# Performance work log

Hardware: AMD Instinct MI355X
Metric: run time of the kernel (lower is better)

## Reference

```python
import jax, jax.numpy as jnp
import numpy as np

B, L, D = 2, 4096, 128      # batch, seq_len, d_model
ED = 2 * D                  # d_inner (expand=2) = 256
N = 16                      # d_state
K = 4                       # d_conv
R = (D + 15) // 16          # dt_rank = 8
H = 2 * D                   # mlp hidden = 256


def setup_inputs() -> dict:
    key = jax.random.key(0)
    ks = jax.random.split(key, 20)
    s = 0.05
    inp = {
        "x": jax.random.normal(ks[0], (B, L, D), dtype=jnp.float32),
        # outer block LayerNorm (norm1)
        "norm1_g": jnp.ones((D,), jnp.float32),
        "norm1_b": jnp.zeros((D,), jnp.float32),
        # MambaLayer inner LayerNorm
        "inner_g": jnp.ones((D,), jnp.float32),
        "inner_b": jnp.zeros((D,), jnp.float32),
        # Mamba params
        "in_w": jax.random.normal(ks[1], (2 * ED, D), jnp.float32) * s,      # in_proj (no bias)
        "conv_w": jax.random.normal(ks[2], (ED, 1, K), jnp.float32) * s,     # depthwise conv
        "conv_b": jax.random.normal(ks[3], (ED,), jnp.float32) * s,
        "xproj_w": jax.random.normal(ks[4], (R + 2 * N, ED), jnp.float32) * s,  # x_proj (no bias)
        "dt_w": jax.random.normal(ks[5], (ED, R), jnp.float32) * s,
        "dt_b": jax.random.normal(ks[6], (ED,), jnp.float32) * s,
        "A_log": jnp.tile(jnp.log(jnp.arange(1, N + 1, dtype=jnp.float32)), (ED, 1)),  # [ED,N]
        "Dp": jnp.ones((ED,), jnp.float32),
        "out_w": jax.random.normal(ks[7], (D, ED), jnp.float32) * s,         # out_proj (no bias)
        # MLP
        "fc1_w": jax.random.normal(ks[8], (H, D), jnp.float32) * s,
        "fc1_b": jnp.zeros((H,), jnp.float32),
        "fc2_w": jax.random.normal(ks[9], (D, H), jnp.float32) * s,
        "fc2_b": jnp.zeros((D,), jnp.float32),
    }
    return inp


def _ln(x, g, b, eps=1e-5):
    m = jnp.mean(x, axis=-1, keepdims=True)
    v = jnp.mean((x - m) ** 2, axis=-1, keepdims=True)
    return (x - m) * jax.lax.rsqrt(v + eps) * g + b


def _mamba(x, in_w, conv_w, conv_b, xproj_w, dt_w, dt_b, A_log, Dp, out_w):
    # x: [B, L, D]
    xz = jnp.einsum('bld,ed->ble', x, in_w)          # [B,L,2*ED]
    u, z = jnp.split(xz, 2, axis=-1)                 # each [B,L,ED]
    # causal depthwise conv1d over L
    u_c = jnp.transpose(u, (0, 2, 1))                # [B,ED,L]
    u_c = jax.lax.conv_general_dilated(
        u_c, conv_w, window_strides=(1,), padding=[(K - 1, 0)],
        dimension_numbers=('NCH', 'OIH', 'NCH'), feature_group_count=ED)
    u = jax.nn.silu(jnp.transpose(u_c, (0, 2, 1)) + conv_b)   # [B,L,ED]
    # input-dependent dt, B, C
    dbc = jnp.einsum('ble,re->blr', u, xproj_w)      # [B,L,R+2N]
    dt, Bm, Cm = jnp.split(dbc, [R, R + N], axis=-1)
    delta = jax.nn.softplus(jnp.einsum('blr,er->ble', dt, dt_w) + dt_b)  # [B,L,ED]
    A = -jnp.exp(A_log)                              # [ED,N]
    deltaA = jnp.exp(jnp.einsum('ble,en->blen', delta, A))               # [B,L,ED,N]
    deltaBu = jnp.einsum('ble,bln,ble->blen', delta, Bm, u)              # [B,L,ED,N]
    # selective scan over L
    def step(h, inp):
        dA, dBu, Ct = inp                            # [B,ED,N],[B,ED,N],[B,N]
        h = dA * h + dBu
        y = jnp.einsum('ben,bn->be', h, Ct)
        return h, y
    h0 = jnp.zeros((B, ED, N), u.dtype)
    xs = (jnp.transpose(deltaA, (1, 0, 2, 3)),
          jnp.transpose(deltaBu, (1, 0, 2, 3)),
          jnp.transpose(Cm, (1, 0, 2)))
    _, ys = jax.lax.scan(step, h0, xs)               # [L,B,ED]
    y = jnp.transpose(ys, (1, 0, 2)) + u * Dp        # [B,L,ED]
    y = y * jax.nn.silu(z)
    return jnp.einsum('ble,de->bld', y, out_w)       # [B,L,D]


def reference(x, norm1_g, norm1_b, inner_g, inner_b, in_w, conv_w, conv_b,
              xproj_w, dt_w, dt_b, A_log, Dp, out_w, fc1_w, fc1_b, fc2_w, fc2_b):
    # attn branch: mamba(inner_LN(norm1(x)))
    a = _mamba(_ln(_ln(x, norm1_g, norm1_b), inner_g, inner_b),
               in_w, conv_w, conv_b, xproj_w, dt_w, dt_b, A_log, Dp, out_w)
    x = x + a
    # mlp branch (note: original applies norm1 again to updated x)
    h = _ln(x, norm1_g, norm1_b)
    h = jax.nn.gelu(jnp.einsum('bld,hd->blh', h, fc1_w) + fc1_b, approximate=False)
    h = jnp.einsum('blh,dh->bld', h, fc2_w) + fc2_b
    return x + h
```

## Files before the change

kernel.cpp:

```cpp
#include <hip/hip_runtime.h>
#include <hip/hip_bf16.h>
#include <math.h>

#define BB 2
#define LL 4096
#define DD 128
#define ED 256
#define NN 16
#define KK 4
#define RR 8
#define HH 256
#define NT (BB*LL)
#define NC 128
#define LC 32

#define LOG2E 1.4426950408889634f

typedef __attribute__((ext_vector_type(8))) short short8;
typedef __attribute__((ext_vector_type(8))) unsigned short ushort8v;
typedef __attribute__((ext_vector_type(4))) float floatx4;

__device__ __forceinline__ unsigned short f2bf(float f) {
  unsigned int b = __builtin_bit_cast(unsigned int, f);
  b += 0x7FFFu + ((b >> 16) & 1u);
  return (unsigned short)(b >> 16);
}

__device__ __forceinline__ float exp2_fast(float x) {
#if __has_builtin(__builtin_amdgcn_exp2f)
  return __builtin_amdgcn_exp2f(x);
#else
  return exp2f(x);
#endif
}

__device__ __forceinline__ ushort8v pack8(const float4& v0, const float4& v1) {
  ushort8v p;
  p[0]=f2bf(v0.x); p[1]=f2bf(v0.y); p[2]=f2bf(v0.z); p[3]=f2bf(v0.w);
  p[4]=f2bf(v1.x); p[5]=f2bf(v1.y); p[6]=f2bf(v1.z); p[7]=f2bf(v1.w);
  return p;
}

__global__ __launch_bounds__(256) void scan1g_k(
    const float* __restrict__ x,
    const float* __restrict__ g1, const float* __restrict__ b1,
    const float* __restrict__ g2, const float* __restrict__ b2,
    const float* __restrict__ in_w,
    const float* __restrict__ cw, const float* __restrict__ cb,
    const float* __restrict__ xpw,
    const float* __restrict__ dtw, const float* __restrict__ dtb,
    const float* __restrict__ A_log,
    float* __restrict__ uc, float* __restrict__ dbc,
    float* __restrict__ delta, float* __restrict__ gate,
    float* __restrict__ cA, float* __restrict__ cH) {
  __shared__ __align__(16) unsigned char SM[69776];
  auto Atile = reinterpret_cast<unsigned short(*)[136]>(SM);
  auto Wch   = reinterpret_cast<unsigned short(*)[136]>(SM);
  auto As    = reinterpret_cast<unsigned short(*)[264]>(SM);
  auto sdel  = reinterpret_cast<float(*)[128]>(SM);
  auto ubuf  = reinterpret_cast<float(*)[257]>(SM + 17408);
  auto Bs    = reinterpret_cast<unsigned short(*)[264]>(SM + 17408);
  auto sdbc  = reinterpret_cast<float(*)[40]>(SM + 17408);
  auto sus   = reinterpret_cast<float(*)[128]>(SM + 53392);

  const int eb = blockIdx.x, c = blockIdx.y, b = blockIdx.z;
  const int tid = threadIdx.x;
  const int t0 = b*LL + c*LC;
  const int wave = tid >> 6, lane = tid & 63;
  const int quad = lane >> 4, l16 = lane & 15;

  {
    const int lr = tid >> 2, lk = (tid & 3) * 32;
    if (lr < 48) {
      if (lr < 35 && !(c == 0 && lr < 3)) {
        const float* Ap = x + (size_t)(t0 - 3 + lr)*DD + lk;
        float4 av[8];
        float s = 0.f, sq = 0.f;
        #pragma unroll
        for (int g = 0; g < 8; g++) {
          av[g] = *(const float4*)(Ap + g*4);
          s  += av[g].x + av[g].y + av[g].z + av[g].w;
          sq += av[g].x*av[g].x + av[g].y*av[g].y + av[g].z*av[g].z + av[g].w*av[g].w;
        }
        s += __shfl_xor(s, 1);  s += __shfl_xor(s, 2);
        sq += __shfl_xor(sq, 1); sq += __shfl_xor(sq, 2);
        const float m1 = s * (1.f/128.f);
        const float rs1 = rsqrtf(sq*(1.f/128.f) - m1*m1 + 1e-5f);
        float s2 = 0.f, sq2 = 0.f;
        #pragma unroll
        for (int g = 0; g < 8; g++) {
          const float4 gg = *(const float4*)(g1 + lk + g*4);
          const float4 bb = *(const float4*)(b1 + lk + g*4);
          av[g].x = (av[g].x - m1)*rs1*gg.x + bb.x;
          av[g].y = (av[g].y - m1)*rs1*gg.y + bb.y;
          av[g].z = (av[g].z - m1)*rs1*gg.z + bb.z;
          av[g].w = (av[g].w - m1)*rs1*gg.w + bb.w;
          s2  += av[g].x + av[g].y + av[g].z + av[g].w;
          sq2 += av[g].x*av[g].x + av[g].y*av[g].y + av[g].z*av[g].z + av[g].w*av[g].w;
        }
        s2 += __shfl_xor(s2, 1);  s2 += __shfl_xor(s2, 2);
        sq2 += __shfl_xor(sq2, 1); sq2 += __shfl_xor(sq2, 2);
        const float m2 = s2 * (1.f/128.f);
        const float rs2 = rsqrtf(sq2*(1.f/128.f) - m2*m2 + 1e-5f);
        #pragma unroll
        for (int g = 0; g < 4; g++) {
          const float4 ga = *(const float4*)(g2 + lk + g*8);
          const float4 gb = *(const float4*)(g2 + lk + g*8 + 4);
          const float4 ba = *(const float4*)(b2 + lk + g*8);
          const float4 bbv= *(const float4*)(b2 + lk + g*8 + 4);
          ushort8v pa;
          pa[0] = f2bf((av[2*g].x   - m2)*rs2*ga.x + ba.x);
          pa[1] = f2bf((av[2*g].y   - m2)*rs2*ga.y + ba.y);
          pa[2] = f2bf((av[2*g].z   - m2)*rs2*ga.z + ba.z);
          pa[3] = f2bf((av[2*g].w   - m2)*rs2*ga.w + ba.w);
          pa[4] = f2bf((av[2*g+1].x - m2)*rs2*gb.x + bbv.x);
          pa[5] = f2bf((av[2*g+1].y - m2)*rs2*gb.y + bbv.y);
          pa[6] = f2bf((av[2*g+1].z - m2)*rs2*gb.z + bbv.z);
          pa[7] = f2bf((av[2*g+1].w - m2)*rs2*gb.w + bbv.w);
          *(ushort8v*)&Atile[lr][lk + g*8] = pa;
        }
      } else {
        const ushort8v zz = {};
        #pragma unroll
        for (int g = 0; g < 4; g++) *(ushort8v*)&Atile[lr][lk + g*8] = zz;
      }
    }
  }
  __syncthreads();

  short8 af[3][4];
  #pragma unroll
  for (int mt = 0; mt < 3; mt++)
    #pragma unroll
    for (int ks = 0; ks < 4; ks++)
      af[mt][ks] = *(const short8*)&Atile[mt*16 + l16][ks*32 + quad*8];
  __syncthreads();

  for (int nc = 0; nc < 6; nc++) {
    const int colbase = (nc < 4) ? nc*64 : 256 + eb*128 + (nc-4)*64;
    {
      const int r = tid >> 2, seg = (tid & 3) * 32;
      const float* wp = in_w + (size_t)(colbase + r)*DD + seg;
      #pragma unroll
      for (int g = 0; g < 4; g++) {
        const float4 v0 = *(const float4*)(wp + g*8);
        const float4 v1 = *(const float4*)(wp + g*8 + 4);
        *(ushort8v*)&Wch[r][seg + g*8] = pack8(v0, v1);
      }
    }
    __syncthreads();
    floatx4 acc[3] = {};
    #pragma unroll
    for (int ks = 0; ks < 4; ks++) {
      short8 bv = *(const short8*)&Wch[wave*16 + l16][ks*32 + quad*8];
      #pragma unroll
      for (int mt = 0; mt < 3; mt++)
        acc[mt] = __builtin_amdgcn_mfma_f32_16x16x32_bf16(af[mt][ks], bv, acc[mt], 0, 0, 0);
    }
    const int coll = wave*16 + l16;
    #pragma unroll
    for (int mt = 0; mt < 3; mt++)
      #pragma unroll
      for (int rr = 0; rr < 4; rr++) {
        const int m = mt*16 + quad*4 + rr;
        if (nc < 4) {
          if (m < 35) ubuf[m][nc*64 + coll] = acc[mt][rr];
        } else {
          if (m >= 3 && m < 35) {
            const float v = acc[mt][rr];
            gate[(size_t)(t0 + m - 3)*ED + (colbase - 256) + coll] =
                v / (1.f + __expf(-v));
          }
        }
      }
    __syncthreads();
  }

  {
    const int ch = tid;
    const float4 w = *(const float4*)(cw + ch*4);
    const float cbe = cb[ch];
    float h0 = ubuf[0][ch], h1 = ubuf[1][ch], h2 = ubuf[2][ch];
    const bool own = (ch >> 7) == eb;
    #pragma unroll
    for (int i = 0; i < LC; i++) {
      const float cur = ubuf[3+i][ch];
      const float a = cbe + h0*w.x + h1*w.y + h2*w.z + cur*w.w;
      const float s = a / (1.f + __expf(-a));
      As[i][ch] = f2bf(s);
      if (own) {
        sus[i][ch & 127] = s;
        uc[(size_t)(t0+i)*ED + ch] = s;
      }
      h0 = h1; h1 = h2; h2 = cur;
    }
  }
  __syncthreads();

  #pragma unroll
  for (int p = 0; p < 8; p++) {
    const int idx = p*256 + tid;
    const int row = idx >> 5;
    const int col = (idx & 31) * 8;
    ushort8v v = {};
    if (row < 40) {
      const float4 v0 = *(const float4*)(xpw + (size_t)row*ED + col);
      const float4 v1 = *(const float4*)(xpw + (size_t)row*ED + col + 4);
      v = pack8(v0, v1);
    }
    *(ushort8v*)&Bs[row][col] = v;
  }
  __syncthreads();

  {
    const int mi = (wave & 1) * 16;
    const int j0 = (wave >> 1) * 2;
    floatx4 acc[2] = {};
    #pragma unroll
    for (int ks = 0; ks < 8; ks++) {
      const int ko = ks*32 + quad*8;
      short8 a  = *(const short8*)&As[mi + l16][ko];
      short8 b0 = *(const short8*)&Bs[j0*16 +      l16][ko];
      short8 b1 = *(const short8*)&Bs[j0*16 + 16 + l16][ko];
      acc[0] = __builtin_amdgcn_mfma_f32_16x16x32_bf16(a, b0, acc[0], 0, 0, 0);
      acc[1] = __builtin_amdgcn_mfma_f32_16x16x32_bf16(a, b1, acc[1], 0, 0, 0);
    }
    __syncthreads();
    #pragma unroll
    for (int f = 0; f < 2; f++) {
      const int n = (j0 + f)*16 + l16;
      #pragma unroll
      for (int r = 0; r < 4; r++) {
        const int m = mi + quad*4 + r;
        if (n < 40) {
          sdbc[m][n] = acc[f][r];
          if (eb == 0) dbc[(size_t)(t0 + m)*40 + n] = acc[f][r];
        }
      }
    }
  }
  __syncthreads();

  const int e_loc = tid >> 1;
  const int half  = tid & 1;
  const int e     = eb*128 + e_loc;
  {
    const float4 w0 = *(const float4*)(dtw + e*RR);
    const float4 w1 = *(const float4*)(dtw + e*RR + 4);
    const float db = dtb[e];
    #pragma unroll 4
    for (int i = 0; i < 16; i++) {
      const int t = half*16 + i;
      const float a = db
          + sdbc[t][0]*w0.x + sdbc[t][1]*w0.y + sdbc[t][2]*w0.z + sdbc[t][3]*w0.w
          + sdbc[t][4]*w1.x + sdbc[t][5]*w1.y + sdbc[t][6]*w1.z + sdbc[t][7]*w1.w;
      const float d = (a > 20.f) ? a : log1pf(__expf(a));
      sdel[t][e_loc] = d;
      delta[(size_t)(t0+t)*ED + e] = d;
    }
  }
  __syncthreads();

  const int n0 = half * 8;
  const float4 a0 = *(const float4*)(A_log + e*NN + n0);
  const float4 a1 = *(const float4*)(A_log + e*NN + n0 + 4);
  float Aen[8] = {-__expf(a0.x)*LOG2E, -__expf(a0.y)*LOG2E,
                  -__expf(a0.z)*LOG2E, -__expf(a0.w)*LOG2E,
                  -__expf(a1.x)*LOG2E, -__expf(a1.y)*LOG2E,
                  -__expf(a1.z)*LOG2E, -__expf(a1.w)*LOG2E};
  float h[8] = {};
  float sumd = 0.f;
  for (int i = 0; i < LC; i++) {
    const float dv = sdel[i][e_loc];
    const float du = dv * sus[i][e_loc];
    const float4 B0 = *(const float4*)&sdbc[i][RR + n0];
    const float4 B1 = *(const float4*)&sdbc[i][RR + n0 + 4];
    const float Bv[8] = {B0.x,B0.y,B0.z,B0.w,B1.x,B1.y,B1.z,B1.w};
    sumd += dv;
    #pragma unroll
    for (int j = 0; j < 8; j++)
      h[j] = exp2_fast(dv * Aen[j])*h[j] + Bv[j]*du;
  }
  const size_t base = (((size_t)c*BB + b)*ED + e)*NN + n0;
  *(float4*)(cA + base)     = make_float4(exp2_fast(sumd*Aen[0]), exp2_fast(sumd*Aen[1]),
                                          exp2_fast(sumd*Aen[2]), exp2_fast(sumd*Aen[3]));
  *(float4*)(cA + base + 4) = make_float4(exp2_fast(sumd*Aen[4]), exp2_fast(sumd*Aen[5]),
                                          exp2_fast(sumd*Aen[6]), exp2_fast(sumd*Aen[7]));
  *(float4*)(cH + base)     = make_float4(h[0], h[1], h[2], h[3]);
  *(float4*)(cH + base + 4) = make_float4(h[4], h[5], h[6], h[7]);
}

__global__ __launch_bounds__(256) void scan2p_k(float* __restrict__ cA,
    const float* __restrict__ cH) {
  const int gt = blockIdx.x*256 + threadIdx.x;
  const int scan = gt >> 2;
  const int seg  = gt & 3;
  const int lane = threadIdx.x & 63;
  const int lb   = lane & ~3;
  const int b = scan >> 12;
  const size_t base = (size_t)b*ED*NN + (scan & 4095);
  const int c0 = seg * 32;

  float ap = 1.f, hs = 0.f;
  for (int g = 0; g < 2; g++) {
    float av[16], hv[16];
    #pragma unroll
    for (int i = 0; i < 16; i++) {
      const size_t idx = (size_t)(c0 + g*16 + i)*(BB*ED*NN) + base;
      av[i] = cA[idx]; hv[i] = cH[idx];
    }
    #pragma unroll
    for (int i = 0; i < 16; i++) {
      hs = av[i]*hs + hv[i];
      ap *= av[i];
    }
  }
  float h = 0.f;
  #pragma unroll
  for (int k = 0; k < 3; k++) {
    const float ak = __shfl(ap, lb + k);
    const float hk = __shfl(hs, lb + k);
    if (seg > k) h = ak*h + hk;
  }
  for (int g = 0; g < 2; g++) {
    float av[16], hv[16];
    #pragma unroll
    for (int i = 0; i < 16; i++) {
      const size_t idx = (size_t)(c0 + g*16 + i)*(BB*ED*NN) + base;
      av[i] = cA[idx]; hv[i] = cH[idx];
    }
    #pragma unroll
    for (int i = 0; i < 16; i++) {
      const size_t idx = (size_t)(c0 + g*16 + i)*(BB*ED*NN) + base;
      cA[idx] = h;
      h = av[i]*h + hv[i];
    }
  }
}

__global__ __launch_bounds__(1024) void tail7_k(
    const float* __restrict__ gate, const float* __restrict__ delta,
    const float* __restrict__ uc, const float* __restrict__ dbc,
    const float* __restrict__ cP, const float* __restrict__ A_log,
    const float* __restrict__ Dpv, const float* __restrict__ x,
    const float* __restrict__ g1, const float* __restrict__ b1,
    const float* __restrict__ out_w, const float* __restrict__ fc1_w,
    const float* __restrict__ fc1_b, const float* __restrict__ fc2_w,
    const float* __restrict__ fc2_b, float* __restrict__ out) {
  __shared__ __align__(16) unsigned short BigW[34816];
  __shared__ __align__(16) unsigned short Au[32][264];
  __shared__ float xs[32][132];
  __shared__ float sbc[32][32];

  const int c = blockIdx.x, b = blockIdx.y;
  const int t0 = b*LL + c*LC;
  const int tid = threadIdx.x;
  const int wave = tid >> 6, lane = tid & 63;
  const int quad = lane >> 4, l16 = lane & 15;

  if (tid < 256) {
    const int row = tid >> 3, c4 = (tid & 7) * 4;
    *(float4*)&sbc[row][c4] = *(const float4*)(dbc + (size_t)(t0 + row)*40 + RR + c4);
  }
  __syncthreads();

  {
    const int r = tid >> 3, k0 = (tid & 7) * 32;
    const float* wp = out_w + (size_t)r*ED + k0;
    #pragma unroll
    for (int g = 0; g < 4; g++) {
      const float4 v0 = *(const float4*)(wp + g*8);
      const float4 v1 = *(const float4*)(wp + g*8 + 4);
      *(ushort8v*)&BigW[(size_t)r*264 + k0 + g*8] = pack8(v0, v1);
    }
  }

  {
    const int e = tid >> 2, q = tid & 3;
    const int n0 = q * 4;
    float Aen[4], h[4];
    {
      const float4 a0 = *(const float4*)(A_log + e*NN + n0);
      Aen[0]=-__expf(a0.x)*LOG2E; Aen[1]=-__expf(a0.y)*LOG2E;
      Aen[2]=-__expf(a0.z)*LOG2E; Aen[3]=-__expf(a0.w)*LOG2E;
      const float4 h0 = *(const float4*)(cP + (((size_t)c*BB + b)*ED + e)*NN + n0);
      h[0]=h0.x; h[1]=h0.y; h[2]=h0.z; h[3]=h0.w;
    }
    const float Dpe = Dpv[e];
    float pd[8], pu[8], pg[8];
    #pragma unroll
    for (int i = 0; i < 8; i++) {
      pd[i] = delta[(size_t)(t0+i)*ED + e];
      pu[i] = uc[(size_t)(t0+i)*ED + e];
      pg[i] = gate[(size_t)(t0+i)*ED + e];
    }
    for (int g4 = 0; g4 < 4; g4++) {
      float cd[8], cu[8], cg[8];
      #pragma unroll
      for (int i = 0; i < 8; i++) { cd[i]=pd[i]; cu[i]=pu[i]; cg[i]=pg[i]; }
      if (g4 < 3) {
        const int tn = t0 + (g4+1)*8;
        #pragma unroll
        for (int i = 0; i < 8; i++) {
          pd[i] = delta[(size_t)(tn+i)*ED + e];
          pu[i] = uc[(size_t)(tn+i)*ED + e];
          pg[i] = gate[(size_t)(tn+i)*ED + e];
        }
      }
      #pragma unroll
      for (int i = 0; i < 8; i++) {
        const int t = g4*8 + i;
        const float dv = cd[i];
        const float uv = cu[i];
        const float du = dv * uv;
        const float4 B0 = *(const float4*)&sbc[t][n0];
        const float4 C0 = *(const float4*)&sbc[t][16 + n0];
        const float Bv[4] = {B0.x,B0.y,B0.z,B0.w};
        const float Cv[4] = {C0.x,C0.y,C0.z,C0.w};
        float part = 0.f;
        #pragma unroll
        for (int j = 0; j < 4; j++) {
          h[j] = exp2_fast(dv * Aen[j])*h[j] + Bv[j]*du;
          part += h[j]*Cv[j];
        }
        part += __shfl_xor(part, 1);
        part += __shfl_xor(part, 2);
        if (q == 0)
          Au[t][e] = f2bf((part + uv*Dpe) * cg[i]);
      }
    }
  }
  __syncthreads();

  {
    const int mi = (wave & 1) * 16;
    const int wn = (wave >> 1) * 16;
    floatx4 acc = {};
    #pragma unroll
    for (int ks = 0; ks < 8; ks++) {
      const int ko = ks*32 + quad*8;
      short8 a  = *(const short8*)&Au[mi + l16][ko];
      short8 bv = *(const short8*)&BigW[(size_t)(wn + l16)*264 + ko];
      acc = __builtin_amdgcn_mfma_f32_16x16x32_bf16(a, bv, acc, 0, 0, 0);
    }
    const int n = wn + l16;
    #pragma unroll
    for (int r = 0; r < 4; r++) {
      const int m = mi + quad*4 + r;
      xs[m][n] = acc[r] + x[(size_t)(t0 + m)*DD + n];
    }
  }
  __syncthreads();

  if (tid < 512) {
    const int lr = tid >> 4, le = (tid & 15) * 8;
    float vv[8];
    float s = 0.f, sq = 0.f;
    #pragma unroll
    for (int i = 0; i < 8; i++) {
      vv[i] = xs[lr][le + i];
      s += vv[i]; sq += vv[i]*vv[i];
    }
    s += __shfl_xor(s, 1);  s += __shfl_xor(s, 2);
    s += __shfl_xor(s, 4);  s += __shfl_xor(s, 8);
    sq += __shfl_xor(sq, 1); sq += __shfl_xor(sq, 2);
    sq += __shfl_xor(sq, 4); sq += __shfl_xor(sq, 8);
    const float mean = s * (1.f/128.f);
    const float rs = rsqrtf(sq*(1.f/128.f) - mean*mean + 1e-5f);
    ushort8v p;
    #pragma unroll
    for (int i = 0; i < 8; i++)
      p[i] = f2bf((vv[i] - mean)*rs*g1[le + i] + b1[le + i]);
    *(ushort8v*)&Au[lr][le] = p;
  }
  {
    const int r = tid >> 2, k0 = (tid & 3) * 32;
    const float* wp = fc1_w + (size_t)r*DD + k0;
    #pragma unroll
    for (int g = 0; g < 4; g++) {
      const float4 v0 = *(const float4*)(wp + g*8);
      const float4 v1 = *(const float4*)(wp + g*8 + 4);
      *(ushort8v*)&BigW[(size_t)r*136 + k0 + g*8] = pack8(v0, v1);
    }
  }
  __syncthreads();

  {
    const int mi = (wave & 1) * 16;
    const int wn = (wave >> 1) * 32;
    floatx4 acc[2] = {};
    #pragma unroll
    for (int ks = 0; ks < 4; ks++) {
      const int ko = ks*32 + quad*8;
      short8 a  = *(const short8*)&Au[mi + l16][ko];
      short8 b0 = *(const short8*)&BigW[(size_t)(wn +      l16)*136 + ko];
      short8 b1 = *(const short8*)&BigW[(size_t)(wn + 16 + l16)*136 + ko];
      acc[0] = __builtin_amdgcn_mfma_f32_16x16x32_bf16(a, b0, acc[0], 0, 0, 0);
      acc[1] = __builtin_amdgcn_mfma_f32_16x16x32_bf16(a, b1, acc[1], 0, 0, 0);
    }
    __syncthreads();
    #pragma unroll
    for (int f = 0; f < 2; f++) {
      const int n = wn + f*16 + l16;
      const float bn = fc1_b[n];
      #pragma unroll
      for (int r = 0; r < 4; r++) {
        const int m = mi + quad*4 + r;
        float v = acc[f][r] + bn;
        v = 0.5f*v*(1.f + erff(v*0.70710678118f));
        Au[m][n] = f2bf(v);
      }
    }
  }
  {
    const int r = tid >> 3, k0 = (tid & 7) * 32;
    const float* wp = fc2_w + (size_t)r*HH + k0;
    #pragma unroll
    for (int g = 0; g < 4; g++) {
      const float4 v0 = *(const float4*)(wp + g*8);
      const float4 v1 = *(const float4*)(wp + g*8 + 4);
      *(ushort8v*)&BigW[(size_t)r*264 + k0 + g*8] = pack8(v0, v1);
    }
  }
  __syncthreads();

  {
    const int mi = (wave & 1) * 16;
    const int wn = (wave >> 1) * 16;
    floatx4 acc = {};
    #pragma unroll
    for (int ks = 0; ks < 8; ks++) {
      const int ko = ks*32 + quad*8;
      short8 a  = *(const short8*)&Au[mi + l16][ko];
      short8 bv = *(const short8*)&BigW[(size_t)(wn + l16)*264 + ko];
      acc = __builtin_amdgcn_mfma_f32_16x16x32_bf16(a, bv, acc, 0, 0, 0);
    }
    const int n = wn + l16;
    const float bn = fc2_b[n];
    #pragma unroll
    for (int r = 0; r < 4; r++) {
      const int m = mi + quad*4 + r;
      out[(size_t)(t0 + m)*DD + n] = acc[r] + bn + xs[m][n];
    }
  }
}

extern "C" void kernel_launch(void* const* d_in, const int* in_sizes, int n_in,
                              void* d_out, int out_size, void* d_ws, size_t ws_size,
                              hipStream_t stream) {
  const float* x      = (const float*)d_in[0];
  const float* n1g    = (const float*)d_in[1];
  const float* n1b    = (const float*)d_in[2];
  const float* ing    = (const float*)d_in[3];
  const float* inb    = (const float*)d_in[4];
  const float* in_w   = (const float*)d_in[5];
  const float* conv_w = (const float*)d_in[6];
  const float* conv_b = (const float*)d_in[7];
  const float* xproj_w= (const float*)d_in[8];
  const float* dt_w   = (const float*)d_in[9];
  const float* dt_b   = (const float*)d_in[10];
  const float* A_log  = (const float*)d_in[11];
  const float* Dpv    = (const float*)d_in[12];
  const float* out_w  = (const float*)d_in[13];
  const float* fc1_w  = (const float*)d_in[14];
  const float* fc1_b  = (const float*)d_in[15];
  const float* fc2_w  = (const float*)d_in[16];
  const float* fc2_b  = (const float*)d_in[17];
  float* out = (float*)d_out;

  float* ws    = (float*)d_ws;
  float* uc    = ws;
  float* dbc   = uc    + (size_t)NT*ED;
  float* delta = dbc   + (size_t)NT*40;
  float* gate  = delta + (size_t)NT*ED;
  float* cA    = gate  + (size_t)NT*ED;
  float* cH    = cA    + (size_t)NC*BB*ED*NN;

  scan1g_k<<<dim3(2, NC, BB), 256, 0, stream>>>(x, n1g, n1b, ing, inb, in_w,
                                                conv_w, conv_b, xproj_w, dt_w, dt_b,
                                                A_log, uc, dbc, delta, gate, cA, cH);
  scan2p_k<<<(4*BB*ED*NN)/256, 256, 0, stream>>>(cA, cH);
  tail7_k<<<dim3(NC, BB), 1024, 0, stream>>>(gate, delta, uc, dbc, cA, A_log, Dpv,
                                             x, n1g, n1b, out_w, fc1_w, fc1_b,
                                             fc2_w, fc2_b, out);
}
```

Before: 166.0 us.

## Merge channel-half blocks into one 512-thread block per chunk in scan phase one

The first scan kernel drops the two-block split over channel halves. One 512-thread block now processes all 256 channels of a chunk, so the in_proj u columns, the LayerNorm, the conv and x_proj are no longer computed twice. The in_proj loop prefetches the next weight tile into registers while the current tile is in use. Conv is done per 64-column tile, and the dt computation is fused into the scan loop. The cost is half as many blocks (256), each with more shared memory, which lowers the parallelism available across the GPU.

```diff
diff --git a/kernel.cpp b/kernel.cpp
--- a/kernel.cpp
+++ b/kernel.cpp
@@ -41,7 +41,7 @@
   return p;
 }
 
-__global__ __launch_bounds__(256) void scan1g_k(
+__global__ __launch_bounds__(512) void scan1h_k(
     const float* __restrict__ x,
     const float* __restrict__ g1, const float* __restrict__ b1,
     const float* __restrict__ g2, const float* __restrict__ b2,
@@ -53,17 +53,16 @@
     float* __restrict__ uc, float* __restrict__ dbc,
     float* __restrict__ delta, float* __restrict__ gate,
     float* __restrict__ cA, float* __restrict__ cH) {
-  __shared__ __align__(16) unsigned char SM[69776];
+  __shared__ __align__(16) unsigned char SM[79888];
   auto Atile = reinterpret_cast<unsigned short(*)[136]>(SM);
-  auto Wch   = reinterpret_cast<unsigned short(*)[136]>(SM);
   auto As    = reinterpret_cast<unsigned short(*)[264]>(SM);
-  auto sdel  = reinterpret_cast<float(*)[128]>(SM);
-  auto ubuf  = reinterpret_cast<float(*)[257]>(SM + 17408);
-  auto Bs    = reinterpret_cast<unsigned short(*)[264]>(SM + 17408);
-  auto sdbc  = reinterpret_cast<float(*)[40]>(SM + 17408);
-  auto sus   = reinterpret_cast<float(*)[128]>(SM + 53392);
-
-  const int eb = blockIdx.x, c = blockIdx.y, b = blockIdx.z;
+  auto Wch   = reinterpret_cast<unsigned short(*)[136]>(SM + 16896);
+  auto Bs    = reinterpret_cast<unsigned short(*)[264]>(SM + 16896);
+  auto ubuf  = reinterpret_cast<float(*)[65]>(SM + 38016);
+  auto sdbc  = reinterpret_cast<float(*)[40]>(SM + 38016);
+  auto sus   = reinterpret_cast<float(*)[256]>(SM + 47120);
+
+  const int c = blockIdx.x, b = blockIdx.y;
   const int tid = threadIdx.x;
   const int t0 = b*LL + c*LC;
   const int wave = tid >> 6, lane = tid & 63;
@@ -128,166 +127,175 @@
   }
   __syncthreads();
 
-  short8 af[3][4];
+  const int nt_w = wave & 3;
+  const int mlo  = (wave < 4) ? 0 : 16;
+  short8 af0[4], af1[4];
   #pragma unroll
-  for (int mt = 0; mt < 3; mt++)
-    #pragma unroll
-    for (int ks = 0; ks < 4; ks++)
-      af[mt][ks] = *(const short8*)&Atile[mt*16 + l16][ks*32 + quad*8];
-  __syncthreads();
-
-  for (int nc = 0; nc < 6; nc++) {
-    const int colbase = (nc < 4) ? nc*64 : 256 + eb*128 + (nc-4)*64;
-    {
-      const int r = tid >> 2, seg = (tid & 3) * 32;
-      const float* wp = in_w + (size_t)(colbase + r)*DD + seg;
+  for (int ks = 0; ks < 4; ks++) {
+    af0[ks] = *(const short8*)&Atile[mlo + l16][ks*32 + quad*8];
+    if (wave < 4) af1[ks] = *(const short8*)&Atile[32 + l16][ks*32 + quad*8];
+  }
+  __syncthreads();
+
+  {
+    const int wr = tid >> 3;
+    const int wseg = (tid & 7) * 16;
+    float4 wv[4];
+    #pragma unroll
+    for (int g = 0; g < 4; g++)
+      wv[g] = *(const float4*)(in_w + (size_t)wr*DD + wseg + g*4);
+    for (int nc = 0; nc < 8; nc++) {
+      *(ushort8v*)&Wch[wr][wseg]     = pack8(wv[0], wv[1]);
+      *(ushort8v*)&Wch[wr][wseg + 8] = pack8(wv[2], wv[3]);
+      __syncthreads();
+      if (nc < 7) {
+        const float* wp = in_w + (size_t)((nc+1)*64 + wr)*DD + wseg;
+        #pragma unroll
+        for (int g = 0; g < 4; g++) wv[g] = *(const float4*)(wp + g*4);
+      }
+      floatx4 acc0 = {}, acc1 = {};
       #pragma unroll
-      for (int g = 0; g < 4; g++) {
-        const float4 v0 = *(const float4*)(wp + g*8);
-        const float4 v1 = *(const float4*)(wp + g*8 + 4);
-        *(ushort8v*)&Wch[r][seg + g*8] = pack8(v0, v1);
-      }
-    }
-    __syncthreads();
-    floatx4 acc[3] = {};
-    #pragma unroll
-    for (int ks = 0; ks < 4; ks++) {
-      short8 bv = *(const short8*)&Wch[wave*16 + l16][ks*32 + quad*8];
-      #pragma unroll
-      for (int mt = 0; mt < 3; mt++)
-        acc[mt] = __builtin_amdgcn_mfma_f32_16x16x32_bf16(af[mt][ks], bv, acc[mt], 0, 0, 0);
-    }
-    const int coll = wave*16 + l16;
-    #pragma unroll
-    for (int mt = 0; mt < 3; mt++)
-      #pragma unroll
-      for (int rr = 0; rr < 4; rr++) {
-        const int m = mt*16 + quad*4 + rr;
-        if (nc < 4) {
-          if (m < 35) ubuf[m][nc*64 + coll] = acc[mt][rr];
-        } else {
-          if (m >= 3 && m < 35) {
-            const float v = acc[mt][rr];
-            gate[(size_t)(t0 + m - 3)*ED + (colbase - 256) + coll] =
-                v / (1.f + __expf(-v));
+      for (int ks = 0; ks < 4; ks++) {
+        short8 bv = *(const short8*)&Wch[nt_w*16 + l16][ks*32 + quad*8];
+        acc0 = __builtin_amdgcn_mfma_f32_16x16x32_bf16(af0[ks], bv, acc0, 0, 0, 0);
+        if (wave < 4)
+          acc1 = __builtin_amdgcn_mfma_f32_16x16x32_bf16(af1[ks], bv, acc1, 0, 0, 0);
+      }
+      const int coll = nt_w*16 + l16;
+      if (nc < 4) {
+        #pragma unroll
+        for (int rr = 0; rr < 4; rr++)
+          ubuf[mlo + quad*4 + rr][coll] = acc0[rr];
+        if (wave < 4) {
+          #pragma unroll
+          for (int rr = 0; rr < 4; rr++) {
+            const int m1 = 32 + quad*4 + rr;
+            if (m1 < 35) ubuf[m1][coll] = acc1[rr];
           }
         }
-      }
-    __syncthreads();
-  }
-
-  {
-    const int ch = tid;
-    const float4 w = *(const float4*)(cw + ch*4);
-    const float cbe = cb[ch];
-    float h0 = ubuf[0][ch], h1 = ubuf[1][ch], h2 = ubuf[2][ch];
-    const bool own = (ch >> 7) == eb;
-    #pragma unroll
-    for (int i = 0; i < LC; i++) {
-      const float cur = ubuf[3+i][ch];
-      const float a = cbe + h0*w.x + h1*w.y + h2*w.z + cur*w.w;
-      const float s = a / (1.f + __expf(-a));
-      As[i][ch] = f2bf(s);
-      if (own) {
-        sus[i][ch & 127] = s;
-        uc[(size_t)(t0+i)*ED + ch] = s;
-      }
-      h0 = h1; h1 = h2; h2 = cur;
+      } else {
+        const int gcol = (nc-4)*64 + coll;
+        #pragma unroll
+        for (int rr = 0; rr < 4; rr++) {
+          const int m0 = mlo + quad*4 + rr;
+          if (m0 >= 3) {
+            const float v = acc0[rr];
+            gate[(size_t)(t0 + m0 - 3)*ED + gcol] = v / (1.f + __expf(-v));
+          }
+        }
+        if (wave < 4) {
+          #pragma unroll
+          for (int rr = 0; rr < 4; rr++) {
+            const int m1 = 32 + quad*4 + rr;
+            if (m1 < 35) {
+              const float v = acc1[rr];
+              gate[(size_t)(t0 + m1 - 3)*ED + gcol] = v / (1.f + __expf(-v));
+            }
+          }
+        }
+      }
+      __syncthreads();
+      if (nc < 4) {
+        const int chl = tid & 63, tg = tid >> 6;
+        const int ch = nc*64 + chl;
+        const float4 w = *(const float4*)(cw + ch*4);
+        const float cbe = cb[ch];
+        float v0 = ubuf[tg*4 + 0][chl];
+        float v1 = ubuf[tg*4 + 1][chl];
+        float v2 = ubuf[tg*4 + 2][chl];
+        #pragma unroll
+        for (int k = 0; k < 4; k++) {
+          const float cur = ubuf[tg*4 + 3 + k][chl];
+          const float a = cbe + v0*w.x + v1*w.y + v2*w.z + cur*w.w;
+          const float s = a / (1.f + __expf(-a));
+          const int i = tg*4 + k;
+          As[i][ch] = f2bf(s);
+          sus[i][ch] = s;
+          uc[(size_t)(t0+i)*ED + ch] = s;
+          v0 = v1; v1 = v2; v2 = cur;
+        }
+      }
     }
   }
   __syncthreads();
 
   #pragma unroll
-  for (int p = 0; p < 8; p++) {
-    const int idx = p*256 + tid;
-    const int row = idx >> 5;
-    const int col = (idx & 31) * 8;
-    ushort8v v = {};
-    if (row < 40) {
+  for (int p = 0; p < 3; p++) {
+    const int idx = p*512 + tid;
+    if (idx < 1280) {
+      const int row = idx >> 5;
+      const int col = (idx & 31) * 8;
       const float4 v0 = *(const float4*)(xpw + (size_t)row*ED + col);
       const float4 v1 = *(const float4*)(xpw + (size_t)row*ED + col + 4);
-      v = pack8(v0, v1);
-    }
-    *(ushort8v*)&Bs[row][col] = v;
-  }
-  __syncthreads();
-
-  {
-    const int mi = (wave & 1) * 16;
-    const int j0 = (wave >> 1) * 2;
-    floatx4 acc[2] = {};
-    #pragma unroll
-    for (int ks = 0; ks < 8; ks++) {
-      const int ko = ks*32 + quad*8;
-      short8 a  = *(const short8*)&As[mi + l16][ko];
-      short8 b0 = *(const short8*)&Bs[j0*16 +      l16][ko];
-      short8 b1 = *(const short8*)&Bs[j0*16 + 16 + l16][ko];
-      acc[0] = __builtin_amdgcn_mfma_f32_16x16x32_bf16(a, b0, acc[0], 0, 0, 0);
-      acc[1] = __builtin_amdgcn_mfma_f32_16x16x32_bf16(a, b1, acc[1], 0, 0, 0);
-    }
-    __syncthreads();
-    #pragma unroll
-    for (int f = 0; f < 2; f++) {
-      const int n = (j0 + f)*16 + l16;
+      *(ushort8v*)&Bs[row][col] = pack8(v0, v1);
+    }
+  }
+  __syncthreads();
+
+  {
+    const int mt = wave & 1, nt = wave >> 1;
+    if (wave < 6) {
+      const int jn = (nt == 2) ? 24 : nt*16;
+      floatx4 acc = {};
       #pragma unroll
-      for (int r = 0; r < 4; r++) {
-        const int m = mi + quad*4 + r;
-        if (n < 40) {
-          sdbc[m][n] = acc[f][r];
-          if (eb == 0) dbc[(size_t)(t0 + m)*40 + n] = acc[f][r];
-        }
-      }
-    }
-  }
-  __syncthreads();
-
-  const int e_loc = tid >> 1;
-  const int half  = tid & 1;
-  const int e     = eb*128 + e_loc;
-  {
-    const float4 w0 = *(const float4*)(dtw + e*RR);
-    const float4 w1 = *(const float4*)(dtw + e*RR + 4);
+      for (int ks = 0; ks < 8; ks++) {
+        const int ko = ks*32 + quad*8;
+        short8 a  = *(const short8*)&As[mt*16 + l16][ko];
+        short8 bv = *(const short8*)&Bs[jn + l16][ko];
+        acc = __builtin_amdgcn_mfma_f32_16x16x32_bf16(a, bv, acc, 0, 0, 0);
+      }
+      const int n = jn + l16;
+      if (nt < 2 || l16 >= 8) {
+        #pragma unroll
+        for (int rr = 0; rr < 4; rr++) {
+          const int m = mt*16 + quad*4 + rr;
+          sdbc[m][n] = acc[rr];
+          dbc[(size_t)(t0 + m)*40 + n] = acc[rr];
+        }
+      }
+    }
+  }
+  __syncthreads();
+
+  {
+    const int e = tid >> 1, half = tid & 1;
+    const int n0 = half * 8;
+    const float4 dw0 = *(const float4*)(dtw + e*RR);
+    const float4 dw1 = *(const float4*)(dtw + e*RR + 4);
     const float db = dtb[e];
-    #pragma unroll 4
-    for (int i = 0; i < 16; i++) {
-      const int t = half*16 + i;
-      const float a = db
-          + sdbc[t][0]*w0.x + sdbc[t][1]*w0.y + sdbc[t][2]*w0.z + sdbc[t][3]*w0.w
-          + sdbc[t][4]*w1.x + sdbc[t][5]*w1.y + sdbc[t][6]*w1.z + sdbc[t][7]*w1.w;
-      const float d = (a > 20.f) ? a : log1pf(__expf(a));
-      sdel[t][e_loc] = d;
-      delta[(size_t)(t0+t)*ED + e] = d;
-    }
-  }
-  __syncthreads();
-
-  const int n0 = half * 8;
-  const float4 a0 = *(const float4*)(A_log + e*NN + n0);
-  const float4 a1 = *(const float4*)(A_log + e*NN + n0 + 4);
-  float Aen[8] = {-__expf(a0.x)*LOG2E, -__expf(a0.y)*LOG2E,
-                  -__expf(a0.z)*LOG2E, -__expf(a0.w)*LOG2E,
-                  -__expf(a1.x)*LOG2E, -__expf(a1.y)*LOG2E,
-                  -__expf(a1.z)*LOG2E, -__expf(a1.w)*LOG2E};
-  float h[8] = {};
-  float sumd = 0.f;
-  for (int i = 0; i < LC; i++) {
-    const float dv = sdel[i][e_loc];
-    const float du = dv * sus[i][e_loc];
-    const float4 B0 = *(const float4*)&sdbc[i][RR + n0];
-    const float4 B1 = *(const float4*)&sdbc[i][RR + n0 + 4];
-    const float Bv[8] = {B0.x,B0.y,B0.z,B0.w,B1.x,B1.y,B1.z,B1.w};
-    sumd += dv;
-    #pragma unroll
-    for (int j = 0; j < 8; j++)
-      h[j] = exp2_fast(dv * Aen[j])*h[j] + Bv[j]*du;
-  }
-  const size_t base = (((size_t)c*BB + b)*ED + e)*NN + n0;
-  *(float4*)(cA + base)     = make_float4(exp2_fast(sumd*Aen[0]), exp2_fast(sumd*Aen[1]),
-                                          exp2_fast(sumd*Aen[2]), exp2_fast(sumd*Aen[3]));
-  *(float4*)(cA + base + 4) = make_float4(exp2_fast(sumd*Aen[4]), exp2_fast(sumd*Aen[5]),
-                                          exp2_fast(sumd*Aen[6]), exp2_fast(sumd*Aen[7]));
-  *(float4*)(cH + base)     = make_float4(h[0], h[1], h[2], h[3]);
-  *(float4*)(cH + base + 4) = make_float4(h[4], h[5], h[6], h[7]);
+    const float4 a0 = *(const float4*)(A_log + e*NN + n0);
+    const float4 a1 = *(const float4*)(A_log + e*NN + n0 + 4);
+    float Aen[8] = {-__expf(a0.x)*LOG2E, -__expf(a0.y)*LOG2E,
+                    -__expf(a0.z)*LOG2E, -__expf(a0.w)*LOG2E,
+                    -__expf(a1.x)*LOG2E, -__expf(a1.y)*LOG2E,
+                    -__expf(a1.z)*LOG2E, -__expf(a1.w)*LOG2E};
+    float h[8] = {};
+    float sumd = 0.f;
+    for (int t = 0; t < LC; t++) {
+      const float4 q0 = *(const float4*)&sdbc[t][0];
+      const float4 q1 = *(const float4*)&sdbc[t][4];
+      const float aa = db
+          + q0.x*dw0.x + q0.y*dw0.y + q0.z*dw0.z + q0.w*dw0.w
+          + q1.x*dw1.x + q1.y*dw1.y + q1.z*dw1.z + q1.w*dw1.w;
+      const float dv = (aa > 20.f) ? aa : log1pf(__expf(aa));
+      if (half == 0) delta[(size_t)(t0+t)*ED + e] = dv;
+      const float du = dv * sus[t][e];
+      const float4 B0 = *(const float4*)&sdbc[t][RR + n0];
+      const float4 B1 = *(const float4*)&sdbc[t][RR + n0 + 4];
+      const float Bv[8] = {B0.x,B0.y,B0.z,B0.w,B1.x,B1.y,B1.z,B1.w};
+      sumd += dv;
+      #pragma unroll
+      for (int j = 0; j < 8; j++)
+        h[j] = exp2_fast(dv * Aen[j])*h[j] + Bv[j]*du;
+    }
+    const size_t base = (((size_t)c*BB + b)*ED + e)*NN + n0;
+    *(float4*)(cA + base)     = make_float4(exp2_fast(sumd*Aen[0]), exp2_fast(sumd*Aen[1]),
+                                            exp2_fast(sumd*Aen[2]), exp2_fast(sumd*Aen[3]));
+    *(float4*)(cA + base + 4) = make_float4(exp2_fast(sumd*Aen[4]), exp2_fast(sumd*Aen[5]),
+                                            exp2_fast(sumd*Aen[6]), exp2_fast(sumd*Aen[7]));
+    *(float4*)(cH + base)     = make_float4(h[0], h[1], h[2], h[3]);
+    *(float4*)(cH + base + 4) = make_float4(h[4], h[5], h[6], h[7]);
+  }
 }
 
 __global__ __launch_bounds__(256) void scan2p_k(float* __restrict__ cA,
@@ -576,9 +584,9 @@
   float* cA    = gate  + (size_t)NT*ED;
   float* cH    = cA    + (size_t)NC*BB*ED*NN;
 
-  scan1g_k<<<dim3(2, NC, BB), 256, 0, stream>>>(x, n1g, n1b, ing, inb, in_w,
-                                                conv_w, conv_b, xproj_w, dt_w, dt_b,
-                                                A_log, uc, dbc, delta, gate, cA, cH);
+  scan1h_k<<<dim3(NC, BB), 512, 0, stream>>>(x, n1g, n1b, ing, inb, in_w,
+                                             conv_w, conv_b, xproj_w, dt_w, dt_b,
+                                             A_log, uc, dbc, delta, gate, cA, cH);
   scan2p_k<<<(4*BB*ED*NN)/256, 256, 0, stream>>>(cA, cH);
   tail7_k<<<dim3(NC, BB), 1024, 0, stream>>>(gate, delta, uc, dbc, cA, A_log, Dpv,
                                              x, n1g, n1b, out_w, fc1_w, fc1_b,
```

Measured after the change: 165.1 us (median of 2 runs). About the same (-0.6%).
